# Kernel optimization log

Measured on AMD Instinct MI355X. Metric: run time of the kernel, lower is better.

Reference implementation:

```python
import jax, jax.numpy as jnp
import numpy as np

N, C, H, W = 32, 64, 128, 128
P_ROLL_H, P_ROLL_W = 1, -2  # frozen values of random.randint(-2, 2) at init

def setup_inputs() -> dict:
    key = jax.random.key(0)
    k1, k2, k3 = jax.random.split(key, 3)
    x = jax.random.normal(k1, (N, C, H, W), dtype=jnp.float32)
    # Conv2d(c, c, (1,7), dilation=(1,3), padding=(0,9), bias=False); torch default kaiming-uniform-ish, use uniform
    fan_in = C * 1 * 7
    bc = 1.0 / np.sqrt(fan_in)
    W_conv = jax.random.uniform(k2, (C, C, 1, 7), minval=-bc, maxval=bc, dtype=jnp.float32)
    # p_4_w: uniform(-sqrt(3/3), sqrt(3/3)) = uniform(-1, 1), shape (3,1)
    p4w = jax.random.uniform(k3, (3, 1), minval=-1.0, maxval=1.0, dtype=jnp.float32)
    return {"x": x, "W_conv": W_conv, "p4w": p4w}

def _dilated_unfold_h(x):
    # F.unfold(x, (3,1), dilation=(2,1), padding=(2,0)) -> (n, c, 3, h, w)
    # tap k gathers row h + 2*(k-1), zero-padded
    xp = jnp.pad(x, ((0, 0), (0, 0), (2, 2), (0, 0)))
    h = x.shape[2]
    return jnp.stack([xp[:, :, 2 * k:2 * k + h, :] for k in range(3)], axis=2)

def reference(x, W_conv, p4w):
    # t_1: dilated 3-tap unfold along h -> (n, c, 3, h, w)
    t1 = _dilated_unfold_h(x)
    # t_2: circular rolls along h and w
    t2 = jnp.roll(jnp.roll(t1, P_ROLL_H, axis=3), P_ROLL_W, axis=4)
    # t_3: conv (1,7) dilation (1,3) pad (0,9), width-preserving
    t3 = jax.lax.conv_general_dilated(
        x, W_conv, window_strides=(1, 1), padding=((0, 0), (9, 9)),
        rhs_dilation=(1, 3), dimension_numbers=("NCHW", "OIHW", "NCHW"))
    # t_4: weighted reduce over the 3 taps (einsum 'abcde,cf->abfde', f=1)
    t4 = jnp.einsum("nckhw,kf->ncfhw", t2, p4w)[:, :, 0]
    # t_6 = (x + conv(x)) * t_4
    return (x + t3) * t4
```

## Files before the change

kernel.cpp:

```cpp
#include <hip/hip_runtime.h>
#include <hip/hip_bf16.h>

#define N_ 32
#define C_ 64
#define H_ 128
#define W_ 128
#define HW_ (H_ * W_)
#define CHW_ (C_ * HW_)

#define XT_STRIDE 72
#define XT_ROWS 146
#define CB_STRIDE 130
#define SMEM_BYTES (4 * 16 * CB_STRIDE * 4)

typedef __bf16 bf16x8 __attribute__((ext_vector_type(8)));
typedef float floatx4 __attribute__((ext_vector_type(4)));

__device__ inline unsigned short f2bf(float f) {
    __hip_bfloat16 h = __float2bfloat16(f);
    return *reinterpret_cast<unsigned short*>(&h);
}

__global__ void prepack_kernel(const float* __restrict__ Wc, uint4* __restrict__ Ap) {
    int idx = blockIdx.x * 256 + threadIdx.x;
    if (idx >= 14 * 4 * 64) return;
    int lane = idx & 63;
    int mt = (idx >> 6) & 3;
    int kt = idx >> 8;
    int m = mt * 16 + (lane & 15);
    int kbase = kt * 32 + (lane >> 4) * 8;
    unsigned int r[4];
    #pragma unroll
    for (int p = 0; p < 4; ++p) {
        unsigned int half[2];
        #pragma unroll
        for (int jj = 0; jj < 2; ++jj) {
            int k = kbase + 2 * p + jj;
            int t = k >> 6;
            int i = k & 63;
            half[jj] = f2bf(Wc[m * 448 + i * 7 + t]);
        }
        r[p] = half[0] | (half[1] << 16);
    }
    Ap[idx] = make_uint4(r[0], r[1], r[2], r[3]);
}

__global__ __launch_bounds__(256) void fused_mfma_kernel(
    const float* __restrict__ x, const uint4* __restrict__ Ap,
    const float* __restrict__ p4w, float* __restrict__ out)
{
    __shared__ __attribute__((aligned(16))) char smem[SMEM_BYTES];
    unsigned short* xT = (unsigned short*)smem;
    float* convbuf = (float*)smem;

    const int b = blockIdx.x;
    const int xcd = b & 7;
    const int i_ = b >> 3;
    const int n = i_ >> 4;
    const int h = xcd * 16 + (i_ & 15);

    const int tid = threadIdx.x;
    const int wave = tid >> 6;
    const int lane = tid & 63;
    const int l16 = lane & 15;
    const int quad = lane >> 4;
    const float* xn = x + (size_t)n * CHW_;

    unsigned int* xz = (unsigned int*)xT;
    for (int i = tid; i < 648; i += 256) {
        int d = (i < 324) ? i : (4932 + (i - 324));
        xz[d] = 0u;
    }

    const float* xrow = xn + h * W_;
    #pragma unroll
    for (int k = 0; k < 8; ++k) {
        int f4 = k * 256 + tid;
        int c = f4 >> 5;
        int w4 = f4 & 31;
        float4 v = *(const float4*)(xrow + c * HW_ + w4 * 4);
        int w = w4 * 4;
        xT[(w + 9) * XT_STRIDE + c]  = f2bf(v.x);
        xT[(w + 10) * XT_STRIDE + c] = f2bf(v.y);
        xT[(w + 11) * XT_STRIDE + c] = f2bf(v.z);
        xT[(w + 12) * XT_STRIDE + c] = f2bf(v.w);
    }

    uint4 afrag[14];
    #pragma unroll
    for (int kt = 0; kt < 14; ++kt)
        afrag[kt] = Ap[kt * 256 + wave * 64 + lane];

    __syncthreads();

    floatx4 acc[8];
    #pragma unroll
    for (int nt = 0; nt < 8; ++nt) acc[nt] = (floatx4){0.f, 0.f, 0.f, 0.f};

    const int base_half = l16 * XT_STRIDE + quad * 8;
    #pragma unroll
    for (int kt = 0; kt < 14; ++kt) {
        bf16x8 av = __builtin_bit_cast(bf16x8, afrag[kt]);
        int koff = (kt >> 1) * 3 * XT_STRIDE + (kt & 1) * 32;
        #pragma unroll
        for (int nt = 0; nt < 8; ++nt) {
            int off = base_half + koff + nt * 16 * XT_STRIDE;
            uint4 d = *(const uint4*)&xT[off];
            bf16x8 bv = __builtin_bit_cast(bf16x8, d);
            acc[nt] = __builtin_amdgcn_mfma_f32_16x16x32_bf16(av, bv, acc[nt], 0, 0, 0);
        }
    }

    __syncthreads();

    float* cw = convbuf + wave * 16 * CB_STRIDE;
    #pragma unroll
    for (int nt = 0; nt < 8; ++nt) {
        #pragma unroll
        for (int r = 0; r < 4; ++r)
            cw[(quad * 4 + r) * CB_STRIDE + nt * 16 + l16] = acc[nt][r];
    }

    const float p0 = p4w[0], p1 = p4w[1], p2 = p4w[2];
    const int h1 = (h - 1 + H_) & 127;

    #pragma unroll
    for (int j = 0; j < 8; ++j) {
        int idx = j * 64 + lane;
        int o_ = idx >> 5;
        int w4 = idx & 31;
        int w = w4 * 4;
        int o = wave * 16 + o_;

        float4 cv = *(const float4*)&cw[o_ * CB_STRIDE + w];

        const float* xc = xn + o * HW_;
        float4 xv = *(const float4*)(xc + h * W_ + w);

        int wsrc = w + 2;
        float tap[3][4];
        #pragma unroll
        for (int k = 0; k < 3; ++k) {
            int hh = h1 + 2 * k - 2;
            if (hh >= 0 && hh < H_) {
                const float* rowp = xc + hh * W_;
                float2 a = *(const float2*)(rowp + wsrc);
                float2 b2 = *(const float2*)(rowp + ((wsrc + 2) & 127));
                tap[k][0] = a.x; tap[k][1] = a.y; tap[k][2] = b2.x; tap[k][3] = b2.y;
            } else {
                tap[k][0] = tap[k][1] = tap[k][2] = tap[k][3] = 0.f;
            }
        }
        float ov[4];
        float xa[4] = {xv.x, xv.y, xv.z, xv.w};
        float ca[4] = {cv.x, cv.y, cv.z, cv.w};
        #pragma unroll
        for (int e = 0; e < 4; ++e) {
            float t4 = p0 * tap[0][e] + p1 * tap[1][e] + p2 * tap[2][e];
            ov[e] = (xa[e] + ca[e]) * t4;
        }
        *(float4*)(out + (size_t)n * CHW_ + o * HW_ + h * W_ + w) =
            make_float4(ov[0], ov[1], ov[2], ov[3]);
    }
}

extern "C" void kernel_launch(void* const* d_in, const int* in_sizes, int n_in,
                              void* d_out, int out_size, void* d_ws, size_t ws_size,
                              hipStream_t stream) {
    const float* x   = (const float*)d_in[0];
    const float* Wc  = (const float*)d_in[1];
    const float* p4w = (const float*)d_in[2];
    float* out       = (float*)d_out;
    uint4* Apack     = (uint4*)d_ws;

    prepack_kernel<<<14, 256, 0, stream>>>(Wc, Apack);
    fused_mfma_kernel<<<N_ * H_, 256, 0, stream>>>(x, Apack, p4w, out);
}
```

Before: 274.2 us.

## Swap MFMA operands to epilogue from registers, swizzle LDS, stream weight fragments

Swaps the MFMA operand roles so the x tile is the A operand and weights are B. Each lane's accumulator then holds four consecutive width positions of one output channel, so the epilogue reads conv results straight from registers. This removes the second barrier and the shared-memory staging of the conv output. The transposed x tile uses an XOR swizzle with packed 2-channel writes to reduce LDS bank conflicts, and weight fragments are prefetched one k-step ahead instead of keeping all 14 in registers. Launch bounds ask for 8 blocks per CU, which may cause spills.

```diff
diff --git a/kernel.cpp b/kernel.cpp
--- a/kernel.cpp
+++ b/kernel.cpp
@@ -10,8 +10,7 @@
 
 #define XT_STRIDE 72
 #define XT_ROWS 146
-#define CB_STRIDE 130
-#define SMEM_BYTES (4 * 16 * CB_STRIDE * 4)
+#define SMEM_HALFS (XT_ROWS * XT_STRIDE)
 
 typedef __bf16 bf16x8 __attribute__((ext_vector_type(8)));
 typedef float floatx4 __attribute__((ext_vector_type(4)));
@@ -45,13 +44,11 @@
     Ap[idx] = make_uint4(r[0], r[1], r[2], r[3]);
 }
 
-__global__ __launch_bounds__(256) void fused_mfma_kernel(
+__global__ __launch_bounds__(256, 8) void fused_mfma_kernel(
     const float* __restrict__ x, const uint4* __restrict__ Ap,
     const float* __restrict__ p4w, float* __restrict__ out)
 {
-    __shared__ __attribute__((aligned(16))) char smem[SMEM_BYTES];
-    unsigned short* xT = (unsigned short*)smem;
-    float* convbuf = (float*)smem;
+    __shared__ __attribute__((aligned(16))) unsigned short xT[SMEM_HALFS];
 
     const int b = blockIdx.x;
     const int xcd = b & 7;
@@ -66,101 +63,112 @@
     const int quad = lane >> 4;
     const float* xn = x + (size_t)n * CHW_;
 
+    const uint4* ApW = Ap + wave * 64 + lane;
+    uint4 bcur = ApW[0];
+
     unsigned int* xz = (unsigned int*)xT;
-    for (int i = tid; i < 648; i += 256) {
-        int d = (i < 324) ? i : (4932 + (i - 324));
-        xz[d] = 0u;
+    #pragma unroll
+    for (int i = 0; i < 3; ++i) {
+        int idx = i * 256 + tid;
+        if (idx < 648) {
+            int d = (idx < 324) ? idx : (4932 + (idx - 324));
+            xz[d] = 0u;
+        }
     }
 
     const float* xrow = xn + h * W_;
+    const int w4 = tid & 31;
+    const int cidx = tid >> 5;
     #pragma unroll
-    for (int k = 0; k < 8; ++k) {
-        int f4 = k * 256 + tid;
-        int c = f4 >> 5;
-        int w4 = f4 & 31;
-        float4 v = *(const float4*)(xrow + c * HW_ + w4 * 4);
-        int w = w4 * 4;
-        xT[(w + 9) * XT_STRIDE + c]  = f2bf(v.x);
-        xT[(w + 10) * XT_STRIDE + c] = f2bf(v.y);
-        xT[(w + 11) * XT_STRIDE + c] = f2bf(v.z);
-        xT[(w + 12) * XT_STRIDE + c] = f2bf(v.w);
+    for (int k = 0; k < 4; ++k) {
+        const int c0 = k * 16 + cidx * 2;
+        const float* pr = xrow + c0 * HW_ + w4 * 4;
+        float4 v0 = *(const float4*)(pr);
+        float4 v1 = *(const float4*)(pr + HW_);
+        const int chunk = c0 >> 3;
+        const int wi = c0 & 7;
+        float a0[4] = {v0.x, v0.y, v0.z, v0.w};
+        float a1[4] = {v1.x, v1.y, v1.z, v1.w};
+        #pragma unroll
+        for (int j = 0; j < 4; ++j) {
+            const int row = w4 * 4 + 9 + j;
+            const int s = (row >> 1) & 7;
+            unsigned int pk = (unsigned int)f2bf(a0[j]) | ((unsigned int)f2bf(a1[j]) << 16);
+            *(unsigned int*)&xT[row * XT_STRIDE + ((chunk ^ s) << 3) + wi] = pk;
+        }
     }
-
-    uint4 afrag[14];
-    #pragma unroll
-    for (int kt = 0; kt < 14; ++kt)
-        afrag[kt] = Ap[kt * 256 + wave * 64 + lane];
 
     __syncthreads();
 
     floatx4 acc[8];
     #pragma unroll
-    for (int nt = 0; nt < 8; ++nt) acc[nt] = (floatx4){0.f, 0.f, 0.f, 0.f};
+    for (int wt = 0; wt < 8; ++wt) acc[wt] = (floatx4){0.f, 0.f, 0.f, 0.f};
 
-    const int base_half = l16 * XT_STRIDE + quad * 8;
     #pragma unroll
     for (int kt = 0; kt < 14; ++kt) {
-        bf16x8 av = __builtin_bit_cast(bf16x8, afrag[kt]);
-        int koff = (kt >> 1) * 3 * XT_STRIDE + (kt & 1) * 32;
+        const int ktn = (kt < 13) ? (kt + 1) : 13;
+        uint4 bnext = ApW[ktn * 256];
+        bf16x8 bv = __builtin_bit_cast(bf16x8, bcur);
+        const int t = kt >> 1;
+        const int row0 = l16 + 3 * t;
+        const int s = (row0 >> 1) & 7;
+        const int cc = (quad ^ s) ^ ((kt & 1) << 2);
+        const unsigned short* pb = &xT[row0 * XT_STRIDE + (cc << 3)];
         #pragma unroll
-        for (int nt = 0; nt < 8; ++nt) {
-            int off = base_half + koff + nt * 16 * XT_STRIDE;
-            uint4 d = *(const uint4*)&xT[off];
-            bf16x8 bv = __builtin_bit_cast(bf16x8, d);
-            acc[nt] = __builtin_amdgcn_mfma_f32_16x16x32_bf16(av, bv, acc[nt], 0, 0, 0);
+        for (int wt = 0; wt < 8; ++wt) {
+            uint4 d = *(const uint4*)(pb + wt * 16 * XT_STRIDE);
+            acc[wt] = __builtin_amdgcn_mfma_f32_16x16x32_bf16(
+                __builtin_bit_cast(bf16x8, d), bv, acc[wt], 0, 0, 0);
         }
-    }
-
-    __syncthreads();
-
-    float* cw = convbuf + wave * 16 * CB_STRIDE;
-    #pragma unroll
-    for (int nt = 0; nt < 8; ++nt) {
-        #pragma unroll
-        for (int r = 0; r < 4; ++r)
-            cw[(quad * 4 + r) * CB_STRIDE + nt * 16 + l16] = acc[nt][r];
+        bcur = bnext;
     }
 
     const float p0 = p4w[0], p1 = p4w[1], p2 = p4w[2];
-    const int h1 = (h - 1 + H_) & 127;
+    const int h1 = (h - 1) & 127;
+    const int o = wave * 16 + l16;
+    const float* xc = xn + (size_t)o * HW_;
+    const float* xh = xc + h * W_;
+    float* oc = out + (size_t)n * CHW_ + (size_t)o * HW_ + h * W_;
+
+    const int hh0 = h1 - 2;
+    const int hh2 = h1 + 2;
+    const bool g0 = (hh0 >= 0);
+    const bool g2 = (hh2 < H_);
+    const float* r0p = xc + hh0 * W_;
+    const float* r1p = xc + h1 * W_;
+    const float* r2p = xc + hh2 * W_;
 
     #pragma unroll
-    for (int j = 0; j < 8; ++j) {
-        int idx = j * 64 + lane;
-        int o_ = idx >> 5;
-        int w4 = idx & 31;
-        int w = w4 * 4;
-        int o = wave * 16 + o_;
+    for (int wt = 0; wt < 8; ++wt) {
+        const int w0 = wt * 16 + quad * 4;
+        float4 xv = *(const float4*)(xh + w0);
+        const int wsa = w0 + 2;
+        const int wsb = (w0 + 4) & 127;
+        float t0[4], t1[4], t2[4];
+        if (g0) {
+            float2 a = *(const float2*)(r0p + wsa);
+            float2 b2 = *(const float2*)(r0p + wsb);
+            t0[0] = a.x; t0[1] = a.y; t0[2] = b2.x; t0[3] = b2.y;
+        } else { t0[0] = t0[1] = t0[2] = t0[3] = 0.f; }
+        {
+            float2 a = *(const float2*)(r1p + wsa);
+            float2 b2 = *(const float2*)(r1p + wsb);
+            t1[0] = a.x; t1[1] = a.y; t1[2] = b2.x; t1[3] = b2.y;
+        }
+        if (g2) {
+            float2 a = *(const float2*)(r2p + wsa);
+            float2 b2 = *(const float2*)(r2p + wsb);
+            t2[0] = a.x; t2[1] = a.y; t2[2] = b2.x; t2[3] = b2.y;
+        } else { t2[0] = t2[1] = t2[2] = t2[3] = 0.f; }
 
-        float4 cv = *(const float4*)&cw[o_ * CB_STRIDE + w];
-
-        const float* xc = xn + o * HW_;
-        float4 xv = *(const float4*)(xc + h * W_ + w);
-
-        int wsrc = w + 2;
-        float tap[3][4];
-        #pragma unroll
-        for (int k = 0; k < 3; ++k) {
-            int hh = h1 + 2 * k - 2;
-            if (hh >= 0 && hh < H_) {
-                const float* rowp = xc + hh * W_;
-                float2 a = *(const float2*)(rowp + wsrc);
-                float2 b2 = *(const float2*)(rowp + ((wsrc + 2) & 127));
-                tap[k][0] = a.x; tap[k][1] = a.y; tap[k][2] = b2.x; tap[k][3] = b2.y;
-            } else {
-                tap[k][0] = tap[k][1] = tap[k][2] = tap[k][3] = 0.f;
-            }
-        }
-        float ov[4];
         float xa[4] = {xv.x, xv.y, xv.z, xv.w};
-        float ca[4] = {cv.x, cv.y, cv.z, cv.w};
+        float rr[4];
         #pragma unroll
         for (int e = 0; e < 4; ++e) {
-            float t4 = p0 * tap[0][e] + p1 * tap[1][e] + p2 * tap[2][e];
-            ov[e] = (xa[e] + ca[e]) * t4;
+            float t4 = p0 * t0[e] + p1 * t1[e] + p2 * t2[e];
+            rr[e] = (xa[e] + acc[wt][e]) * t4;
         }
-        *(float4*)(out + (size_t)n * CHW_ + o * HW_ + h * W_ + w) =
-            make_float4(ov[0], ov[1], ov[2], ov[3]);
+        *(float4*)(oc + w0) = make_float4(rr[0], rr[1], rr[2], rr[3]);
     }
 }
 
```

New measurement: 333.5 us. 21.6% more time.
